# Kernel tuning notes

Hardware: AMD Instinct MI355X
Metric: run time of the kernel (lower is better)

Reference implementation:

```python
import jax, jax.numpy as jnp
import numpy as np
from jax import lax

B, C, H, W = 2, 192, 256, 256
HEADS = 6
QC = 4 * C  # elementwise gate: q, gate, k, v
EPS = 1e-12


def setup_inputs() -> dict:
    key = jax.random.key(0)
    ks = jax.random.split(key, 8)
    x = jax.random.normal(ks[0], (B, C, H, W), dtype=jnp.float32)
    qkv_w = jax.random.normal(ks[1], (QC, C), dtype=jnp.float32) * (1.0 / np.sqrt(C))
    qkv_b = jax.random.normal(ks[2], (QC,), dtype=jnp.float32) * 0.02
    dw_w = jax.random.normal(ks[3], (QC, 1, 3, 3), dtype=jnp.float32) * (1.0 / 3.0)
    dw_b = jax.random.normal(ks[4], (QC,), dtype=jnp.float32) * 0.02
    temperature = jnp.ones((HEADS, 1, 1), dtype=jnp.float32)
    proj_w = jax.random.normal(ks[5], (C, C), dtype=jnp.float32) * (1.0 / np.sqrt(C))
    proj_b = jax.random.normal(ks[6], (C,), dtype=jnp.float32) * 0.02
    return {"x": x, "qkv_w": qkv_w, "qkv_b": qkv_b, "dw_w": dw_w, "dw_b": dw_b,
            "temperature": temperature, "proj_w": proj_w, "proj_b": proj_b}


def reference(x, qkv_w, qkv_b, dw_w, dw_b, temperature, proj_w, proj_b):
    b, c, h, w = x.shape
    hd = c // HEADS  # head_dim
    n = h * w
    # 1x1 conv qkv projection
    qkv = jnp.einsum('bchw,oc->bohw', x, qkv_w) + qkv_b[None, :, None, None]
    # 3x3 depthwise conv (groups == channels)
    qkv = lax.conv_general_dilated(
        qkv, dw_w, window_strides=(1, 1), padding=((1, 1), (1, 1)),
        dimension_numbers=('NCHW', 'OIHW', 'NCHW'), feature_group_count=QC)
    qkv = qkv + dw_b[None, :, None, None]
    # split: q, gate (elementwise), k, v
    q = qkv[:, :c]
    gate = qkv[:, c:2 * c]
    k = qkv[:, 2 * c:3 * c]
    v = qkv[:, 3 * c:]
    # b (head c) h w -> b head c (h w)
    def to_heads(t):
        return t.reshape(b, HEADS, hd, n)
    q, k, v, gate = to_heads(q), to_heads(k), to_heads(v), to_heads(gate)
    # L2 normalize along token dim (matches F.normalize eps clamp)
    q = q / jnp.maximum(jnp.sqrt(jnp.sum(q * q, axis=-1, keepdims=True)), EPS)
    k = k / jnp.maximum(jnp.sqrt(jnp.sum(k * k, axis=-1, keepdims=True)), EPS)
    # channel attention: [b, head, hd, hd]
    attn = jnp.einsum('bhcn,bhdn->bhcd', q, k) * temperature[None]
    attn = jax.nn.softmax(attn, axis=-1)
    out = jnp.einsum('bhcd,bhdn->bhcn', attn, v)
    out = out * jax.nn.sigmoid(gate)
    out = out.reshape(b, c, h, w)
    out = jnp.einsum('bchw,oc->bohw', out, proj_w) + proj_b[None, :, None, None]
    return out
```

## Files before the change

kernel.cpp:

```cpp
#include <hip/hip_runtime.h>
#include <math.h>


#define HEADS 6
#define CDIM 192
#define QCH 768
#define HH 256
#define WW 256
#define NPIX 65536
#define PADC 200

typedef __bf16 bf16x8 __attribute__((ext_vector_type(8)));
typedef float f32x4 __attribute__((ext_vector_type(4)));
typedef unsigned short u16x8 __attribute__((ext_vector_type(8)));

__device__ __forceinline__ float b2f(unsigned short u) {
  union { unsigned int i; float f; } x; x.i = ((unsigned int)u) << 16; return x.f;
}
__device__ __forceinline__ unsigned short f2b(float f) {
  union { float f; unsigned int i; } x; x.f = f;
  unsigned int lsb = (x.i >> 16) & 1u;
  x.i += 0x7fffu + lsb;
  return (unsigned short)(x.i >> 16);
}

__global__ void zero_init(float* __restrict__ p, int n) {
  int i = blockIdx.x * 256 + threadIdx.x;
  if (i < n) p[i] = 0.f;
}

__global__ __launch_bounds__(256)
void w2bf(const float* __restrict__ qkv_w, const float* __restrict__ proj_w,
          unsigned short* __restrict__ wbf) {
  int id = blockIdx.x * 256 + threadIdx.x;
  if (id >= 5 * 192 * 192) return;
  int k = id % 192;
  int m = (id / 192) % 192;
  int q = id / (192 * 192);
  float v = (q < 4) ? qkv_w[(size_t)(q * 192 + m) * 192 + k]
                    : proj_w[(size_t)m * 192 + k];
  wbf[((size_t)q * 192 + m) * PADC + k] = f2b(v);
}

__global__ __launch_bounds__(256)
void x2t(const float* __restrict__ x, unsigned short* __restrict__ xT) {
  __shared__ unsigned short tile[64 * PADC];
  int t = threadIdx.x;
  int n0 = blockIdx.x * 64;
  int b = blockIdx.y;
  #pragma unroll
  for (int i = 0; i < 12; ++i) {
    int idx = t + i * 256;
    int c = idx >> 4;
    int nn4 = (idx & 15) << 2;
    float4 v = *(const float4*)(x + ((size_t)b * CDIM + c) * NPIX + n0 + nn4);
    tile[(nn4 + 0) * PADC + c] = f2b(v.x);
    tile[(nn4 + 1) * PADC + c] = f2b(v.y);
    tile[(nn4 + 2) * PADC + c] = f2b(v.z);
    tile[(nn4 + 3) * PADC + c] = f2b(v.w);
  }
  __syncthreads();
  #pragma unroll
  for (int i = 0; i < 6; ++i) {
    int idx = t + i * 256;
    int row = idx / 24;
    int c8 = (idx % 24) * 8;
    *(u16x8*)(xT + ((size_t)b * NPIX + n0 + row) * PADC + c8) =
        *(const u16x8*)(tile + row * PADC + c8);
  }
}

template <int NMT>
__global__ __launch_bounds__(256)
void gemm_t(const unsigned short* __restrict__ wq0,
            const unsigned short* __restrict__ wq1,
            const float* __restrict__ bias0,
            const float* __restrict__ bias1,
            const unsigned short* __restrict__ Bsrc,
            unsigned short* __restrict__ outB)
{
  __shared__ unsigned short a_lds[64 * PADC];
  __shared__ unsigned short b_lds[64 * PADC];
  int t = threadIdx.x;
  int n0 = blockIdx.x * 64;
  int b = blockIdx.y;

  const unsigned short* Bs = Bsrc + ((size_t)b * NPIX + n0) * PADC;
  #pragma unroll
  for (int i = 0; i < 6; ++i) {
    int idx = t + i * 256;
    *(u16x8*)(b_lds + idx * 8) = *(const u16x8*)(Bs + (size_t)idx * 8);
  }
  if (t < 64) {
    int idx = 1536 + t;
    *(u16x8*)(b_lds + idx * 8) = *(const u16x8*)(Bs + (size_t)idx * 8);
  }

  int wid = t >> 6, lane = t & 63;
  int r = lane & 15, quad = lane >> 4;

  #pragma unroll
  for (int mt = 0; mt < NMT; ++mt) {
    int half = mt / 3;
    int mrow = (mt % 3) * 64;
    const unsigned short* wq = (half ? wq1 : wq0) + (size_t)mrow * PADC;

    __syncthreads();
    #pragma unroll
    for (int i = 0; i < 6; ++i) {
      int idx = t + i * 256;
      *(u16x8*)(a_lds + idx * 8) = *(const u16x8*)(wq + (size_t)idx * 8);
    }
    if (t < 64) {
      int idx = 1536 + t;
      *(u16x8*)(a_lds + idx * 8) = *(const u16x8*)(wq + (size_t)idx * 8);
    }
    __syncthreads();

    f32x4 acc[4];
    #pragma unroll
    for (int nt = 0; nt < 4; ++nt) acc[nt] = (f32x4){0.f, 0.f, 0.f, 0.f};

    #pragma unroll
    for (int kk = 0; kk < 192; kk += 32) {
      bf16x8 xf = *(const bf16x8*)(b_lds + (wid * 16 + r) * PADC + kk + quad * 8);
      #pragma unroll
      for (int nt = 0; nt < 4; ++nt) {
        bf16x8 wf = *(const bf16x8*)(a_lds + (nt * 16 + r) * PADC + kk + quad * 8);
        acc[nt] = __builtin_amdgcn_mfma_f32_16x16x32_bf16(xf, wf, acc[nt], 0, 0, 0);
      }
    }

    const float* bp = half ? bias1 : bias0;
    size_t n = (size_t)n0 + wid * 16 + quad * 4;
    unsigned short* op = outB + (size_t)(b * 2 + half) * CDIM * NPIX;
    #pragma unroll
    for (int nt = 0; nt < 4; ++nt) {
      int m = mrow + nt * 16 + r;
      float bb = bp[m];
      ushort4 uu;
      uu.x = f2b(acc[nt][0] + bb); uu.y = f2b(acc[nt][1] + bb);
      uu.z = f2b(acc[nt][2] + bb); uu.w = f2b(acc[nt][3] + bb);
      *(ushort4*)(op + (size_t)m * NPIX + n) = uu;
    }
  }
}

__global__ __launch_bounds__(256)
void proj_fused(const unsigned short* __restrict__ wproj,
                const float* __restrict__ bias,
                const unsigned short* __restrict__ post2,
                const unsigned short* __restrict__ Pbf,
                float* __restrict__ out)
{
  __shared__ unsigned short a_lds[64 * PADC];
  __shared__ unsigned short b_lds[64 * PADC];
  int t = threadIdx.x;
  int n0 = blockIdx.x * 64;
  int b = blockIdx.y;
  int wid = t >> 6, lane = t & 63;
  int r = lane & 15, quad = lane >> 4;
  int nl = wid * 16 + r;
  size_t n = (size_t)n0 + nl;

  const unsigned short* vbase = post2 + (size_t)(b * 2 + 0) * CDIM * NPIX;
  const unsigned short* gbase = post2 + (size_t)(b * 2 + 1) * CDIM * NPIX;
  const unsigned short* Pb = Pbf + (size_t)b * HEADS * 1024;

  #pragma unroll
  for (int h = 0; h < HEADS; ++h) {
    union { unsigned short u[8]; bf16x8 v; } vf;
    #pragma unroll
    for (int j = 0; j < 8; ++j)
      vf.u[j] = vbase[(size_t)(h * 32 + quad * 8 + j) * NPIX + n];
    #pragma unroll
    for (int c0 = 0; c0 < 32; c0 += 16) {
      bf16x8 pf = *(const bf16x8*)(Pb + h * 1024 + (c0 + r) * 32 + quad * 8);
      f32x4 d = (f32x4){0.f, 0.f, 0.f, 0.f};
      d = __builtin_amdgcn_mfma_f32_16x16x32_bf16(pf, vf.v, d, 0, 0, 0);
      #pragma unroll
      for (int i = 0; i < 4; ++i) {
        int c = c0 + quad * 4 + i;
        float gg = b2f(gbase[(size_t)(h * 32 + c) * NPIX + n]);
        float sg = 1.f / (1.f + expf(-gg));
        b_lds[nl * PADC + h * 32 + c] = f2b(d[i] * sg);
      }
    }
  }

  #pragma unroll
  for (int mt = 0; mt < 3; ++mt) {
    int mrow = mt * 64;
    const unsigned short* wq = wproj + (size_t)mrow * PADC;

    __syncthreads();
    #pragma unroll
    for (int i = 0; i < 6; ++i) {
      int idx = t + i * 256;
      *(u16x8*)(a_lds + idx * 8) = *(const u16x8*)(wq + (size_t)idx * 8);
    }
    if (t < 64) {
      int idx = 1536 + t;
      *(u16x8*)(a_lds + idx * 8) = *(const u16x8*)(wq + (size_t)idx * 8);
    }
    __syncthreads();

    f32x4 acc[4];
    #pragma unroll
    for (int nt = 0; nt < 4; ++nt) acc[nt] = (f32x4){0.f, 0.f, 0.f, 0.f};

    #pragma unroll
    for (int kk = 0; kk < 192; kk += 32) {
      bf16x8 xf = *(const bf16x8*)(b_lds + (wid * 16 + r) * PADC + kk + quad * 8);
      #pragma unroll
      for (int nt = 0; nt < 4; ++nt) {
        bf16x8 wf = *(const bf16x8*)(a_lds + (nt * 16 + r) * PADC + kk + quad * 8);
        acc[nt] = __builtin_amdgcn_mfma_f32_16x16x32_bf16(xf, wf, acc[nt], 0, 0, 0);
      }
    }

    size_t nn = (size_t)n0 + wid * 16 + quad * 4;
    float* op = out + (size_t)b * CDIM * NPIX;
    #pragma unroll
    for (int nt = 0; nt < 4; ++nt) {
      int m = mrow + nt * 16 + r;
      float bb = bias[m];
      float4 vv;
      vv.x = acc[nt][0] + bb; vv.y = acc[nt][1] + bb;
      vv.z = acc[nt][2] + bb; vv.w = acc[nt][3] + bb;
      *(float4*)(op + (size_t)m * NPIX + nn) = vv;
    }
  }
}

__global__ __launch_bounds__(256)
void dwconv_ssq(const unsigned short* __restrict__ in,
                const float* __restrict__ w9,
                const float* __restrict__ bias,
                unsigned short* __restrict__ outp,
                float* __restrict__ ssqBase,
                int qs0, int qs1)
{
  __shared__ unsigned short lds[34][256];
  __shared__ float red[4];
  int t = threadIdx.x;
  int z = blockIdx.z;
  int qsel = (z & 1) ? qs1 : qs0;
  int o  = blockIdx.x >> 3;
  int ry = blockIdx.x & 7;
  int y0 = ry << 5;

  const unsigned short* base = in + ((size_t)z * CDIM + o) * NPIX;
  #pragma unroll
  for (int i = 0; i < 9; ++i) {
    int idx = t + i * 256;
    if (idx < 2176) {
      int row = idx >> 6;
      int c4  = (idx & 63) << 2;
      int gy  = y0 - 1 + row;
      ushort4 vv = make_ushort4(0, 0, 0, 0);
      if (gy >= 0 && gy < HH)
        vv = *(const ushort4*)(base + (size_t)gy * WW + c4);
      *(ushort4*)(&lds[row][c4]) = vv;
    }
  }

  float wv[9];
  #pragma unroll
  for (int i = 0; i < 9; ++i) wv[i] = w9[((size_t)qsel * CDIM + o) * 9 + i];
  float bo = bias[qsel * CDIM + o];
  __syncthreads();

  int w = t >> 6, lane = t & 63;
  int x0 = lane << 2;
  float sumsq = 0.f;
  unsigned short* outbase = outp + ((size_t)z * CDIM + o) * NPIX;

  #pragma unroll
  for (int i = 0; i < 8; ++i) {
    int yo = w * 8 + i;
    float a0 = bo, a1 = bo, a2 = bo, a3 = bo;
    #pragma unroll
    for (int dy = 0; dy < 3; ++dy) {
      ushort4 mv = *(const ushort4*)(&lds[yo + dy][x0]);
      float v0 = b2f(mv.x), v1 = b2f(mv.y), v2 = b2f(mv.z), v3 = b2f(mv.w);
      float vl = __shfl_up(v3, 1, 64);   if (lane == 0)  vl = 0.f;
      float vr = __shfl_down(v0, 1, 64); if (lane == 63) vr = 0.f;
      float w0 = wv[dy * 3 + 0], w1 = wv[dy * 3 + 1], w2 = wv[dy * 3 + 2];
      a0 += w0 * vl + w1 * v0 + w2 * v1;
      a1 += w0 * v0 + w1 * v1 + w2 * v2;
      a2 += w0 * v1 + w1 * v2 + w2 * v3;
      a3 += w0 * v2 + w1 * v3 + w2 * vr;
    }
    ushort4 ov;
    ov.x = f2b(a0); ov.y = f2b(a1); ov.z = f2b(a2); ov.w = f2b(a3);
    *(ushort4*)(outbase + (size_t)(y0 + yo) * WW + x0) = ov;
    if (ssqBase != nullptr) sumsq += a0 * a0 + a1 * a1 + a2 * a2 + a3 * a3;
  }

  if (ssqBase != nullptr) {
    float* ssq = ssqBase + (size_t)(z >> 1) * 2 * CDIM + (z & 1) * CDIM;
    #pragma unroll
    for (int off = 32; off; off >>= 1) sumsq += __shfl_down(sumsq, off, 64);
    if (lane == 0) red[w] = sumsq;
    __syncthreads();
    if (t == 0) atomicAdd(&ssq[o], red[0] + red[1] + red[2] + red[3]);
  }
}

__global__ __launch_bounds__(256)
void gram(const unsigned short* __restrict__ post,
          float* __restrict__ S)
{
  int h = blockIdx.y, b = blockIdx.z;
  int t = threadIdx.x, wid = t >> 6, lane = t & 63;
  int r = lane & 15, quad = lane >> 4;
  int c0 = (wid >> 1) * 16, d0 = (wid & 1) * 16;
  size_t nb = (size_t)blockIdx.x * 512 + quad * 8;
  const unsigned short* qrow =
      post + ((size_t)(b * 2 + 0) * CDIM + h * 32 + c0 + r) * NPIX + nb;
  const unsigned short* krow =
      post + ((size_t)(b * 2 + 1) * CDIM + h * 32 + d0 + r) * NPIX + nb;
  f32x4 acc = (f32x4){0.f, 0.f, 0.f, 0.f};
  #pragma unroll
  for (int kk = 0; kk < 512; kk += 32) {
    bf16x8 af  = *(const bf16x8*)(qrow + kk);
    bf16x8 bfr = *(const bf16x8*)(krow + kk);
    acc = __builtin_amdgcn_mfma_f32_16x16x32_bf16(af, bfr, acc, 0, 0, 0);
  }
  float* Sp = S + ((size_t)b * HEADS + h) * 1024;
  #pragma unroll
  for (int i = 0; i < 4; ++i)
    atomicAdd(&Sp[(c0 + quad * 4 + i) * 32 + (d0 + r)], acc[i]);
}

__global__ void softmax_scale(const float* __restrict__ S,
                              const float* __restrict__ ssq,
                              const float* __restrict__ temp,
                              unsigned short* __restrict__ Pbf)
{
  int h = blockIdx.x, b = blockIdx.y;
  int t = threadIdx.x;
  int c = t >> 5, d = t & 31;
  float nq = fmaxf(sqrtf(ssq[(size_t)b * 2 * CDIM + h * 32 + c]), 1e-12f);
  float nk = fmaxf(sqrtf(ssq[(size_t)b * 2 * CDIM + CDIM + h * 32 + d]), 1e-12f);
  float v = S[((size_t)b * HEADS + h) * 1024 + t] / (nq * nk) * temp[h];
  float m = v;
  for (int off = 16; off; off >>= 1) m = fmaxf(m, __shfl_xor(m, off, 32));
  float e = expf(v - m);
  float s = e;
  for (int off = 16; off; off >>= 1) s += __shfl_xor(s, off, 32);
  Pbf[((size_t)b * HEADS + h) * 1024 + c * 32 + d] = f2b(e / s);
}

extern "C" void kernel_launch(void* const* d_in, const int* in_sizes, int n_in,
                              void* d_out, int out_size, void* d_ws, size_t ws_size,
                              hipStream_t stream)
{
  const float* x      = (const float*)d_in[0];
  const float* qkv_w  = (const float*)d_in[1];
  const float* qkv_b  = (const float*)d_in[2];
  const float* dw_w   = (const float*)d_in[3];
  const float* dw_b   = (const float*)d_in[4];
  const float* temp   = (const float*)d_in[5];
  const float* proj_w = (const float*)d_in[6];
  const float* proj_b = (const float*)d_in[7];
  float* out = (float*)d_out;

  char* ws = (char*)d_ws;
  const size_t qbytes  = (size_t)CDIM * NPIX * 2;
  const size_t xTbytes = (size_t)2 * NPIX * PADC * 2;
  const size_t wbytes  = (size_t)5 * 192 * PADC * 2;
  unsigned short* xT    = (unsigned short*)ws;
  unsigned short* wbf   = (unsigned short*)(ws + xTbytes);
  unsigned short* pre   = (unsigned short*)(ws + xTbytes + wbytes);
  unsigned short* post  = (unsigned short*)(ws + xTbytes + wbytes + 4 * qbytes);
  unsigned short* post2 = (unsigned short*)(ws + xTbytes + wbytes + 8 * qbytes);
  float* S   = (float*)(ws + xTbytes + wbytes + 12 * qbytes);
  float* ssq = S + 2 * HEADS * 1024;
  unsigned short* Pbf = (unsigned short*)(ssq + 2 * 2 * CDIM);
  const int nz = 2 * HEADS * 1024 + 2 * 2 * CDIM;

  zero_init<<<(nz + 255) / 256, 256, 0, stream>>>(S, nz);
  w2bf<<<(5 * 192 * 192 + 255) / 256, 256, 0, stream>>>(qkv_w, proj_w, wbf);
  x2t<<<dim3(NPIX / 64, 2), 256, 0, stream>>>(x, xT);

  const unsigned short* wq = wbf;
  const size_t wqs = (size_t)192 * PADC;

  gemm_t<6><<<dim3(NPIX / 64, 2), 256, 0, stream>>>(
      wq + 0 * wqs, wq + 2 * wqs, qkv_b + 0 * CDIM, qkv_b + 2 * CDIM, xT, pre);
  dwconv_ssq<<<dim3(CDIM * 8, 1, 4), 256, 0, stream>>>(pre, dw_w, dw_b, post, ssq, 0, 2);

  gemm_t<6><<<dim3(NPIX / 64, 2), 256, 0, stream>>>(
      wq + 3 * wqs, wq + 1 * wqs, qkv_b + 3 * CDIM, qkv_b + 1 * CDIM, xT, pre);
  dwconv_ssq<<<dim3(CDIM * 8, 1, 4), 256, 0, stream>>>(pre, dw_w, dw_b, post2, nullptr, 3, 1);

  gram<<<dim3(128, HEADS, 2), 256, 0, stream>>>(post, S);
  softmax_scale<<<dim3(HEADS, 2), 1024, 0, stream>>>(S, ssq, temp, Pbf);

  proj_fused<<<dim3(NPIX / 64, 2), 256, 0, stream>>>(
      wq + 4 * wqs, proj_b, post2, Pbf, out);
}
```

Baseline: 507.3 us.

## Keep GEMM weights in registers and stream pixel tiles per block

The qkv GEMM kernel is restructured so that each block owns one 64-row weight tile, held in registers, and loops over four pixel tiles. Previously each block loaded one pixel tile and looped over six weight tiles through LDS. This removes the weight LDS staging and its loads, but the x tile is now re-read from global memory six times, once per weight tile, instead of once. Separately, the sigmoid in the projection kernel switches to the fast __expf intrinsic.

```diff
diff --git a/kernel.cpp b/kernel.cpp
--- a/kernel.cpp
+++ b/kernel.cpp
@@ -9,6 +9,7 @@
 #define WW 256
 #define NPIX 65536
 #define PADC 200
+#define GNT 4
 
 typedef __bf16 bf16x8 __attribute__((ext_vector_type(8)));
 typedef float f32x4 __attribute__((ext_vector_type(4)));
@@ -70,7 +71,6 @@
   }
 }
 
-template <int NMT>
 __global__ __launch_bounds__(256)
 void gemm_t(const unsigned short* __restrict__ wq0,
             const unsigned short* __restrict__ wq1,
@@ -79,41 +79,41 @@
             const unsigned short* __restrict__ Bsrc,
             unsigned short* __restrict__ outB)
 {
-  __shared__ unsigned short a_lds[64 * PADC];
   __shared__ unsigned short b_lds[64 * PADC];
   int t = threadIdx.x;
-  int n0 = blockIdx.x * 64;
-  int b = blockIdx.y;
-
-  const unsigned short* Bs = Bsrc + ((size_t)b * NPIX + n0) * PADC;
-  #pragma unroll
-  for (int i = 0; i < 6; ++i) {
-    int idx = t + i * 256;
-    *(u16x8*)(b_lds + idx * 8) = *(const u16x8*)(Bs + (size_t)idx * 8);
-  }
-  if (t < 64) {
-    int idx = 1536 + t;
-    *(u16x8*)(b_lds + idx * 8) = *(const u16x8*)(Bs + (size_t)idx * 8);
-  }
-
+  int mt = blockIdx.y;
+  int half = mt / 3;
+  int mrow = (mt % 3) * 64;
+  int b = blockIdx.z;
   int wid = t >> 6, lane = t & 63;
   int r = lane & 15, quad = lane >> 4;
 
-  #pragma unroll
-  for (int mt = 0; mt < NMT; ++mt) {
-    int half = mt / 3;
-    int mrow = (mt % 3) * 64;
-    const unsigned short* wq = (half ? wq1 : wq0) + (size_t)mrow * PADC;
-
-    __syncthreads();
+  const unsigned short* wq = (half ? wq1 : wq0) + (size_t)mrow * PADC;
+  bf16x8 wreg[4][6];
+  #pragma unroll
+  for (int nt = 0; nt < 4; ++nt) {
+    #pragma unroll
+    for (int k6 = 0; k6 < 6; ++k6)
+      wreg[nt][k6] = *(const bf16x8*)(wq + (size_t)(nt * 16 + r) * PADC + k6 * 32 + quad * 8);
+  }
+  const float* bp = half ? bias1 : bias0;
+  float bb[4];
+  #pragma unroll
+  for (int nt = 0; nt < 4; ++nt) bb[nt] = bp[mrow + nt * 16 + r];
+
+  unsigned short* op = outB + (size_t)(b * 2 + half) * CDIM * NPIX;
+
+  for (int ni = 0; ni < GNT; ++ni) {
+    int n0 = (blockIdx.x * GNT + ni) * 64;
+    const unsigned short* Bs = Bsrc + ((size_t)b * NPIX + n0) * PADC;
     #pragma unroll
     for (int i = 0; i < 6; ++i) {
       int idx = t + i * 256;
-      *(u16x8*)(a_lds + idx * 8) = *(const u16x8*)(wq + (size_t)idx * 8);
+      *(u16x8*)(b_lds + idx * 8) = *(const u16x8*)(Bs + (size_t)idx * 8);
     }
     if (t < 64) {
       int idx = 1536 + t;
-      *(u16x8*)(a_lds + idx * 8) = *(const u16x8*)(wq + (size_t)idx * 8);
+      *(u16x8*)(b_lds + idx * 8) = *(const u16x8*)(Bs + (size_t)idx * 8);
     }
     __syncthreads();
 
@@ -122,27 +122,23 @@
     for (int nt = 0; nt < 4; ++nt) acc[nt] = (f32x4){0.f, 0.f, 0.f, 0.f};
 
     #pragma unroll
-    for (int kk = 0; kk < 192; kk += 32) {
-      bf16x8 xf = *(const bf16x8*)(b_lds + (wid * 16 + r) * PADC + kk + quad * 8);
+    for (int k6 = 0; k6 < 6; ++k6) {
+      bf16x8 xf = *(const bf16x8*)(b_lds + (wid * 16 + r) * PADC + k6 * 32 + quad * 8);
       #pragma unroll
-      for (int nt = 0; nt < 4; ++nt) {
-        bf16x8 wf = *(const bf16x8*)(a_lds + (nt * 16 + r) * PADC + kk + quad * 8);
-        acc[nt] = __builtin_amdgcn_mfma_f32_16x16x32_bf16(xf, wf, acc[nt], 0, 0, 0);
-      }
-    }
-
-    const float* bp = half ? bias1 : bias0;
+      for (int nt = 0; nt < 4; ++nt)
+        acc[nt] = __builtin_amdgcn_mfma_f32_16x16x32_bf16(xf, wreg[nt][k6], acc[nt], 0, 0, 0);
+    }
+
     size_t n = (size_t)n0 + wid * 16 + quad * 4;
-    unsigned short* op = outB + (size_t)(b * 2 + half) * CDIM * NPIX;
     #pragma unroll
     for (int nt = 0; nt < 4; ++nt) {
       int m = mrow + nt * 16 + r;
-      float bb = bp[m];
       ushort4 uu;
-      uu.x = f2b(acc[nt][0] + bb); uu.y = f2b(acc[nt][1] + bb);
-      uu.z = f2b(acc[nt][2] + bb); uu.w = f2b(acc[nt][3] + bb);
+      uu.x = f2b(acc[nt][0] + bb[nt]); uu.y = f2b(acc[nt][1] + bb[nt]);
+      uu.z = f2b(acc[nt][2] + bb[nt]); uu.w = f2b(acc[nt][3] + bb[nt]);
       *(ushort4*)(op + (size_t)m * NPIX + n) = uu;
     }
+    __syncthreads();
   }
 }
 
@@ -182,7 +178,7 @@
       for (int i = 0; i < 4; ++i) {
         int c = c0 + quad * 4 + i;
         float gg = b2f(gbase[(size_t)(h * 32 + c) * NPIX + n]);
-        float sg = 1.f / (1.f + expf(-gg));
+        float sg = 1.f / (1.f + __expf(-gg));
         b_lds[nl * PADC + h * 32 + c] = f2b(d[i] * sg);
       }
     }
@@ -224,10 +220,10 @@
     #pragma unroll
     for (int nt = 0; nt < 4; ++nt) {
       int m = mrow + nt * 16 + r;
-      float bb = bias[m];
+      float bbv = bias[m];
       float4 vv;
-      vv.x = acc[nt][0] + bb; vv.y = acc[nt][1] + bb;
-      vv.z = acc[nt][2] + bb; vv.w = acc[nt][3] + bb;
+      vv.x = acc[nt][0] + bbv; vv.y = acc[nt][1] + bbv;
+      vv.z = acc[nt][2] + bbv; vv.w = acc[nt][3] + bbv;
       *(float4*)(op + (size_t)m * NPIX + nn) = vv;
     }
   }
@@ -388,11 +384,11 @@
   const unsigned short* wq = wbf;
   const size_t wqs = (size_t)192 * PADC;
 
-  gemm_t<6><<<dim3(NPIX / 64, 2), 256, 0, stream>>>(
+  gemm_t<<<dim3(NPIX / (64 * GNT), 6, 2), 256, 0, stream>>>(
       wq + 0 * wqs, wq + 2 * wqs, qkv_b + 0 * CDIM, qkv_b + 2 * CDIM, xT, pre);
   dwconv_ssq<<<dim3(CDIM * 8, 1, 4), 256, 0, stream>>>(pre, dw_w, dw_b, post, ssq, 0, 2);
 
-  gemm_t<6><<<dim3(NPIX / 64, 2), 256, 0, stream>>>(
+  gemm_t<<<dim3(NPIX / (64 * GNT), 6, 2), 256, 0, stream>>>(
       wq + 3 * wqs, wq + 1 * wqs, qkv_b + 3 * CDIM, qkv_b + 1 * CDIM, xT, pre);
   dwconv_ssq<<<dim3(CDIM * 8, 1, 4), 256, 0, stream>>>(pre, dw_w, dw_b, post2, nullptr, 3, 1);
 
```

Result: no change. 512.4 us (+1.0%).
